# Performance work log

Hardware: AMD Instinct MI355X
Metric: run time of the kernel (lower is better)

Reference implementation:

```python
import jax, jax.numpy as jnp
import numpy as np

B, NE, NMAX = 256, 90, 270
ZE = PE = GE = PPS = 32
NPROPS = 20
FP, SGE, LATH = 256, 64, 128
PIN = FP + SGE + LATH  # 448 = pred_inp_size = conv input (add_to_node)
C1, C2, H = 448, 256, 3
P1 = P2 = 512
EPS = 1e-5

PNAMES = ['sg_emb_table','lat_W1','lat_b1','lat_bn1_g','lat_bn1_b','lat_bn1_m','lat_bn1_v',
          'lat_W2','lat_b2','lat_bn2_g','lat_bn2_b','lat_bn2_m','lat_bn2_v',
          'z_emb_table','period_table','group_table','props','W_props','b_props','W_phys','b_phys',
          'gat1_W','gat1_as','gat1_ad','gat1_b','gat2_W','gat2_as','gat2_ad','gat2_b',
          'pW1','pb1','pbn1_g','pbn1_b','pbn1_m','pbn1_v',
          'pW2','pb2','pbn2_g','pbn2_b','pbn2_m','pbn2_v','pW3','pb3']

def _bn(x, g, b, m, v):
    return (x - m) * g / jnp.sqrt(v + EPS) + b

def _lrelu(x, s=0.2):
    return jnp.where(x >= 0, x, s * x)

def _gat(x, adj, W, a_s, a_d, bias):
    # PyG DenseGATConv: concat=False (mean over heads), dropout=0, negative_slope=0.2
    Bn, N, _ = x.shape
    h = (x @ W).reshape(Bn, N, H, -1)                      # [B,N,H,C]
    asrc = (h * a_s).sum(-1)                               # [B,N,H]
    adst = (h * a_d).sum(-1)
    alpha = asrc[:, None, :, :] + adst[:, :, None, :]      # [B,i,j,H]
    alpha = _lrelu(alpha, 0.2)
    adj_sl = jnp.maximum(adj, jnp.eye(N, dtype=adj.dtype))  # add self loops
    alpha = jnp.where(adj_sl[..., None] > 0, alpha, -jnp.inf)
    alpha = jax.nn.softmax(alpha, axis=2)                  # softmax over sources j
    out = jnp.einsum('bijh,bjhc->bihc', alpha, h)
    return out.mean(2) + bias                              # [B,N,C]

def _forward(comp, sg, lat, period_idx, group_idx, p):
    sg_x = p['sg_emb_table'][sg[:, 0]]                     # [B,SGE]
    # lattice MLP: (Linear -> BN -> LeakyReLU(True)==identity) x2
    h = _bn(lat @ p['lat_W1'] + p['lat_b1'], p['lat_bn1_g'], p['lat_bn1_b'], p['lat_bn1_m'], p['lat_bn1_v'])
    lat_x = _bn(h @ p['lat_W2'] + p['lat_b2'], p['lat_bn2_g'], p['lat_bn2_b'], p['lat_bn2_m'], p['lat_bn2_v'])
    # ragged -> dense batch: expand composition counts into dense node-type grid
    n_atoms = comp.sum(1)                                  # [B]
    cum = jnp.cumsum(comp, axis=1)                         # [B,NE]
    t = jnp.arange(NMAX)
    z = jax.vmap(lambda c: jnp.searchsorted(c, t, side='right'))(cum)  # [B,NMAX]
    mask = t[None, :] < n_atoms[:, None]                   # [B,NMAX] valid nodes
    z = jnp.where(mask, z, 0)
    # PhysEmbedding: z/period/group embeddings + projected properties -> final proj
    phys = jnp.concatenate([
        p['z_emb_table'][z],
        p['period_table'][period_idx[z]],
        p['group_table'][group_idx[z]],
        p['props'][z] @ p['W_props'] + p['b_props'],
    ], axis=-1)
    phys = phys @ p['W_phys'] + p['b_phys']                # [B,NMAX,FP]
    # add_to_node: cat graph-level lat/sg embeddings onto every node, then zero-pad
    node = jnp.concatenate([
        phys,
        jnp.broadcast_to(lat_x[:, None, :], (lat_x.shape[0], NMAX, LATH)),
        jnp.broadcast_to(sg_x[:, None, :], (sg_x.shape[0], NMAX, SGE)),
    ], axis=-1)
    node = node * mask[..., None].astype(node.dtype)       # to_dense_batch zero padding
    # per-graph dense block adjacency, zero diagonal (fill_diagonal_(0))
    adj = (mask[:, :, None] & mask[:, None, :]).astype(node.dtype)
    adj = adj * (1.0 - jnp.eye(NMAX, dtype=node.dtype))
    # GNNBlock: act = LeakyReLU(True) == identity (negative_slope=1)
    x1 = _gat(node, adj, p['gat1_W'], p['gat1_as'], p['gat1_ad'], p['gat1_b'])
    x2 = _gat(x1, adj, p['gat2_W'], p['gat2_as'], p['gat2_ad'], p['gat2_b'])
    comp_x = x2.sum(1)                                     # sum over ALL NMAX slots (incl. padding, as torch does)
    feat = jnp.concatenate([comp_x, sg_x, lat_x], axis=-1) # [B,PIN]
    # prediction head (eval: dropout off, BN running stats)
    h = _lrelu(_bn(feat @ p['pW1'] + p['pb1'], p['pbn1_g'], p['pbn1_b'], p['pbn1_m'], p['pbn1_v']))
    h = _lrelu(_bn(h @ p['pW2'] + p['pb2'], p['pbn2_g'], p['pbn2_b'], p['pbn2_m'], p['pbn2_v']))
    return h @ p['pW3'] + p['pb3']                         # [B,1]

def setup_inputs():
    key = jax.random.key(0)
    ks = iter(jax.random.split(key, 64))
    def nrm(shape, s=0.05):
        return jax.random.normal(next(ks), shape, dtype=jnp.float32) * s
    comp = jax.random.randint(next(ks), (B, NE), 0, 4, dtype=jnp.int32)
    comp = comp.at[0].set(3)  # graph 0 has exactly NMAX atoms -> data N_max == NMAX
    sg = jax.random.randint(next(ks), (B, 1), 0, 230)
    lat = jax.random.uniform(next(ks), (B, 6), dtype=jnp.float32)
    period_idx = jax.random.randint(next(ks), (NE,), 0, 8)
    group_idx = jax.random.randint(next(ks), (NE,), 0, 19)
    inp = dict(comp=comp, sg=sg, lat=lat, period_idx=period_idx, group_idx=group_idx)
    inp.update(
        sg_emb_table=nrm((230, SGE)),
        lat_W1=nrm((6, LATH)), lat_b1=nrm((LATH,)),
        lat_bn1_g=jnp.ones(LATH), lat_bn1_b=jnp.zeros(LATH), lat_bn1_m=jnp.zeros(LATH), lat_bn1_v=jnp.ones(LATH),
        lat_W2=nrm((LATH, LATH)), lat_b2=nrm((LATH,)),
        lat_bn2_g=jnp.ones(LATH), lat_bn2_b=jnp.zeros(LATH), lat_bn2_m=jnp.zeros(LATH), lat_bn2_v=jnp.ones(LATH),
        z_emb_table=nrm((NE, ZE)), period_table=nrm((8, PE)), group_table=nrm((19, GE)),
        props=nrm((NE, NPROPS), 0.1), W_props=nrm((NPROPS, PPS)), b_props=nrm((PPS,)),
        W_phys=nrm((ZE + PE + GE + PPS, FP)), b_phys=nrm((FP,)),
        gat1_W=nrm((PIN, H * C1)), gat1_as=nrm((H, C1)), gat1_ad=nrm((H, C1)), gat1_b=nrm((C1,)),
        gat2_W=nrm((C1, H * C2)), gat2_as=nrm((H, C2)), gat2_ad=nrm((H, C2)), gat2_b=nrm((C2,)),
        pW1=nrm((PIN, P1)), pb1=nrm((P1,)),
        pbn1_g=jnp.ones(P1), pbn1_b=jnp.zeros(P1), pbn1_m=jnp.zeros(P1), pbn1_v=jnp.ones(P1),
        pW2=nrm((P1, P2)), pb2=nrm((P2,)),
        pbn2_g=jnp.ones(P2), pbn2_b=jnp.zeros(P2), pbn2_m=jnp.zeros(P2), pbn2_v=jnp.ones(P2),
        pW3=nrm((P2, 1)), pb3=nrm((1,)),
    )
    return inp

def reference(comp, sg, lat, period_idx, group_idx,
              sg_emb_table, lat_W1, lat_b1, lat_bn1_g, lat_bn1_b, lat_bn1_m, lat_bn1_v,
              lat_W2, lat_b2, lat_bn2_g, lat_bn2_b, lat_bn2_m, lat_bn2_v,
              z_emb_table, period_table, group_table, props, W_props, b_props, W_phys, b_phys,
              gat1_W, gat1_as, gat1_ad, gat1_b, gat2_W, gat2_as, gat2_ad, gat2_b,
              pW1, pb1, pbn1_g, pbn1_b, pbn1_m, pbn1_v,
              pW2, pb2, pbn2_g, pbn2_b, pbn2_m, pbn2_v, pW3, pb3):
    vals = (sg_emb_table, lat_W1, lat_b1, lat_bn1_g, lat_bn1_b, lat_bn1_m, lat_bn1_v,
            lat_W2, lat_b2, lat_bn2_g, lat_bn2_b, lat_bn2_m, lat_bn2_v,
            z_emb_table, period_table, group_table, props, W_props, b_props, W_phys, b_phys,
            gat1_W, gat1_as, gat1_ad, gat1_b, gat2_W, gat2_as, gat2_ad, gat2_b,
            pW1, pb1, pbn1_g, pbn1_b, pbn1_m, pbn1_v,
            pW2, pb2, pbn2_g, pbn2_b, pbn2_m, pbn2_v, pW3, pb3)
    p = dict(zip(PNAMES, vals))
    return _forward(comp, sg, lat, period_idx, group_idx, p)
```

## Files before the change

kernel.cpp:

```cpp
#include <hip/hip_runtime.h>
#include <math.h>

#define BB 256
#define NEL 90
#define NMAX 270
#define C1 448
#define C2 256
#define PIN 448
#define LATH 128
#define SGE 64
#define P1 512
#define EPSB 1e-5f

typedef short shortx8 __attribute__((ext_vector_type(8)));
typedef float floatx4 __attribute__((ext_vector_type(4)));

__device__ __forceinline__ float bf2f(unsigned short u) {
  return __uint_as_float(((unsigned)u) << 16);
}
__device__ __forceinline__ unsigned short f2bf(float f) {
  unsigned x = __float_as_uint(f);
  unsigned r = (x + 0x7fffu + ((x >> 16) & 1u)) >> 16;
  return (unsigned short)r;
}
__device__ __forceinline__ void gld16(const void* g, void* l) {
  __builtin_amdgcn_global_load_lds(
      (const __attribute__((address_space(1))) unsigned int*)g,
      (__attribute__((address_space(3))) unsigned int*)l, 16, 0, 0);
}

__global__ __launch_bounds__(256) void k_prep(
    const int* __restrict__ comp, const int* __restrict__ sg, const float* __restrict__ lat,
    const float* __restrict__ sg_emb,
    const float* __restrict__ W1, const float* __restrict__ b1,
    const float* __restrict__ g1, const float* __restrict__ be1,
    const float* __restrict__ m1, const float* __restrict__ v1,
    const float* __restrict__ W2, const float* __restrict__ b2,
    const float* __restrict__ g2, const float* __restrict__ be2,
    const float* __restrict__ m2, const float* __restrict__ v2,
    float* __restrict__ sgx, float* __restrict__ latx,
    int* __restrict__ z, int* __restrict__ natoms) {
  int b = blockIdx.x;
  int tid = threadIdx.x;
  __shared__ int cum[NEL];
  __shared__ float hbuf[LATH];
  __shared__ float latl[6];
  if (tid == 0) {
    int s = 0;
    for (int e = 0; e < NEL; ++e) { s += comp[b * NEL + e]; cum[e] = s; }
    natoms[b] = s;
  }
  if (tid < 6) latl[tid] = lat[b * 6 + tid];
  __syncthreads();
  int n = cum[NEL - 1];
  for (int t = tid; t < NMAX; t += blockDim.x) {
    int zz = -1;
    if (t < n) {
      for (int e = 0; e < NEL; ++e) { if (cum[e] > t) { zz = e; break; } }
    }
    z[b * NMAX + t] = zz;
  }
  if (tid < SGE) {
    int si = sg[b];
    sgx[b * SGE + tid] = sg_emb[si * SGE + tid];
  }
  if (tid < LATH) {
    float acc = b1[tid];
    for (int k = 0; k < 6; ++k) acc += latl[k] * W1[k * LATH + tid];
    acc = (acc - m1[tid]) * g1[tid] * rsqrtf(v1[tid] + EPSB) + be1[tid];
    hbuf[tid] = acc;
  }
  __syncthreads();
  if (tid < LATH) {
    float acc = b2[tid];
    for (int k = 0; k < LATH; ++k) acc += hbuf[k] * W2[k * LATH + tid];
    acc = (acc - m2[tid]) * g2[tid] * rsqrtf(v2[tid] + EPSB) + be2[tid];
    latx[b * LATH + tid] = acc;
  }
}

__global__ __launch_bounds__(256) void k_scan(const int* __restrict__ natoms,
                                              int* __restrict__ off,
                                              int* __restrict__ aoff,
                                              float* __restrict__ zerobuf) {
  __shared__ int sh[BB];
  int tid = threadIdx.x;
  zerobuf[tid] = 0.f;
  int v0 = natoms[tid];
  sh[tid] = v0;
  for (int d = 1; d < BB; d <<= 1) {
    __syncthreads();
    int v = (tid >= d) ? sh[tid - d] : 0;
    __syncthreads();
    sh[tid] += v;
  }
  __syncthreads();
  off[tid] = sh[tid] - v0;
  __syncthreads();
  int sz = 3 * ((((v0 + 15) >> 4) << 4)) * ((((v0 + 31) >> 5) << 5));
  sh[tid] = sz;
  for (int d = 1; d < BB; d <<= 1) {
    __syncthreads();
    int v = (tid >= d) ? sh[tid - d] : 0;
    __syncthreads();
    sh[tid] += v;
  }
  __syncthreads();
  aoff[tid] = sh[tid] - sz;
}

__global__ __launch_bounds__(256) void k_physpe(
    const int* __restrict__ period_idx, const int* __restrict__ group_idx,
    const float* __restrict__ z_emb, const float* __restrict__ period_t,
    const float* __restrict__ group_t, const float* __restrict__ props,
    const float* __restrict__ Wp, const float* __restrict__ bp,
    const float* __restrict__ Wphys, const float* __restrict__ bphys,
    float* __restrict__ physpe) {
  int e = blockIdx.x;
  int tid = threadIdx.x;
  __shared__ float ph[128];
  if (tid < 32) ph[tid] = z_emb[e * 32 + tid];
  else if (tid < 64) ph[tid] = period_t[period_idx[e] * 32 + tid - 32];
  else if (tid < 96) ph[tid] = group_t[group_idx[e] * 32 + tid - 64];
  else if (tid < 128) {
    int j = tid - 96;
    float acc = bp[j];
    for (int k = 0; k < 20; ++k) acc += props[e * 20 + k] * Wp[k * 32 + j];
    ph[tid] = acc;
  }
  __syncthreads();
  float acc = bphys[tid];
  for (int k = 0; k < 128; ++k) acc += ph[k] * Wphys[k * 256 + tid];
  physpe[e * 256 + tid] = acc;
}

__global__ __launch_bounds__(256) void k_nodep(
    const int* __restrict__ z, const int* __restrict__ off, const int* __restrict__ natoms,
    const float* __restrict__ physpe, const float* __restrict__ latx,
    const float* __restrict__ sgx, unsigned short* __restrict__ x0) {
  int b = blockIdx.x;
  int n = natoms[b], ob = off[b];
  int tid = threadIdx.x;
  __shared__ int zl[NMAX];
  for (int t = tid; t < n; t += 256) zl[t] = z[b * NMAX + t];
  __syncthreads();
  int items = n * 56;
  for (int e = tid; e < items; e += 256) {
    int t = e / 56, c8 = (e - t * 56) << 3;
    int zt = zl[t];
    float v[8];
    if (c8 < 256) {
      float4 a = *(const float4*)(physpe + zt * 256 + c8);
      float4 c = *(const float4*)(physpe + zt * 256 + c8 + 4);
      v[0] = a.x; v[1] = a.y; v[2] = a.z; v[3] = a.w;
      v[4] = c.x; v[5] = c.y; v[6] = c.z; v[7] = c.w;
    } else if (c8 < 384) {
      float4 a = *(const float4*)(latx + b * LATH + c8 - 256);
      float4 c = *(const float4*)(latx + b * LATH + c8 - 252);
      v[0] = a.x; v[1] = a.y; v[2] = a.z; v[3] = a.w;
      v[4] = c.x; v[5] = c.y; v[6] = c.z; v[7] = c.w;
    } else {
      float4 a = *(const float4*)(sgx + b * SGE + c8 - 384);
      float4 c = *(const float4*)(sgx + b * SGE + c8 - 380);
      v[0] = a.x; v[1] = a.y; v[2] = a.z; v[3] = a.w;
      v[4] = c.x; v[5] = c.y; v[6] = c.z; v[7] = c.w;
    }
    unsigned short u[8];
    #pragma unroll
    for (int i = 0; i < 8; ++i) u[i] = f2bf(v[i]);
    *(uint4*)(x0 + (size_t)(ob + t) * PIN + c8) = *(uint4*)u;
  }
}

__global__ __launch_bounds__(256) void k_wprep(
    const float* __restrict__ W, unsigned short* __restrict__ Wt, int K, int NC3) {
  int k0 = blockIdx.x << 5;
  int c0 = blockIdx.y << 5;
  __shared__ float ts[32][33];
  int e = threadIdx.x << 2;
  int kk = e >> 5, cc = e & 31;
  float4 v = *(const float4*)(W + (size_t)(k0 + kk) * NC3 + c0 + cc);
  ts[kk][cc] = v.x; ts[kk][cc + 1] = v.y; ts[kk][cc + 2] = v.z; ts[kk][cc + 3] = v.w;
  __syncthreads();
  int c2 = threadIdx.x & 31, kg = threadIdx.x >> 5;
  ushort4 u;
  u.x = f2bf(ts[kg * 4 + 0][c2]); u.y = f2bf(ts[kg * 4 + 1][c2]);
  u.z = f2bf(ts[kg * 4 + 2][c2]); u.w = f2bf(ts[kg * 4 + 3][c2]);
  *(ushort4*)(Wt + (size_t)(c0 + c2) * K + k0 + (kg << 2)) = u;
}

__global__ __launch_bounds__(64) void k_fold(
    const float* __restrict__ W, const float* __restrict__ a_s, const float* __restrict__ a_d,
    int NC3, int C, float* __restrict__ wsv, float* __restrict__ wdv) {
  int k = blockIdx.x;
  int tid = threadIdx.x;
  for (int h = 0; h < 3; ++h) {
    float ss = 0.f, sd = 0.f;
    for (int c = tid; c < C; c += 64) {
      float wv = W[(size_t)k * NC3 + h * C + c];
      ss += wv * a_s[h * C + c];
      sd += wv * a_d[h * C + c];
    }
    for (int o = 32; o > 0; o >>= 1) { ss += __shfl_down(ss, o); sd += __shfl_down(sd, o); }
    if (tid == 0) { wsv[k * 3 + h] = ss; wdv[k * 3 + h] = sd; }
  }
}

__global__ __launch_bounds__(256) void k_av2(
    const unsigned short* __restrict__ x, const float* __restrict__ wsv,
    const float* __restrict__ wdv, const int* __restrict__ off,
    const int* __restrict__ natoms, float* __restrict__ asrc,
    float* __restrict__ adst, int K) {
  __shared__ float sw[C1 * 3], dw[C1 * 3];
  int tid = threadIdx.x;
  for (int e = tid; e < K * 3; e += 256) { sw[e] = wsv[e]; dw[e] = wdv[e]; }
  __syncthreads();
  int total = off[BB - 1] + natoms[BB - 1];
  int row = blockIdx.x * 256 + tid;
  if (row >= total) return;
  const unsigned short* xr = x + (size_t)row * K;
  float s0 = 0.f, s1 = 0.f, s2 = 0.f, d0 = 0.f, d1 = 0.f, d2 = 0.f;
  for (int k = 0; k < K; k += 8) {
    uint4 raw = *(const uint4*)(xr + k);
    unsigned short us[8];
    *(uint4*)us = raw;
    #pragma unroll
    for (int u = 0; u < 8; ++u) {
      float xv = bf2f(us[u]);
      int kb = (k + u) * 3;
      s0 += xv * sw[kb + 0]; s1 += xv * sw[kb + 1]; s2 += xv * sw[kb + 2];
      d0 += xv * dw[kb + 0]; d1 += xv * dw[kb + 1]; d2 += xv * dw[kb + 2];
    }
  }
  asrc[row * 3 + 0] = s0; asrc[row * 3 + 1] = s1; asrc[row * 3 + 2] = s2;
  adst[row * 3 + 0] = d0; adst[row * 3 + 1] = d1; adst[row * 3 + 2] = d2;
}

#define MTMAX 17
__global__ __launch_bounds__(256) void k_alpha(
    const float* __restrict__ asrc, const float* __restrict__ adst,
    const int* __restrict__ off, const int* __restrict__ natoms,
    const int* __restrict__ aoff, unsigned short* __restrict__ alpha) {
  int bid = blockIdx.x;
  int b = bid & (BB - 1);
  int hm = bid >> 8;
  int h = hm % 3;
  int mt = hm / 3;
  int n = natoms[b];
  if (n == 0) return;
  int mtn = (n + 15) >> 4;
  if (mt >= mtn) return;
  int ktn = (n + 31) >> 5;
  int rext = mtn << 4, kext = ktn << 5;
  int ob = off[b];
  size_t ab = (size_t)aoff[b] + (size_t)h * rext * kext;
  int tid = threadIdx.x;
  int wv = tid >> 6, lane = tid & 63;
  __shared__ float asl[288];
  for (int j = tid; j < kext; j += 256)
    asl[j] = (j < n) ? asrc[(ob + j) * 3 + h] : 0.f;
  __syncthreads();
  #pragma unroll
  for (int r = 0; r < 4; ++r) {
    int i = (mt << 4) + (wv << 2) + r;
    unsigned short* rowp = alpha + ab + (size_t)i * kext;
    if (i >= n) {
      for (int j = lane; j < kext; j += 64) rowp[j] = 0;
      continue;
    }
    float ad = adst[(ob + i) * 3 + h];
    float m = -1e30f;
    for (int j = lane; j < n; j += 64) {
      float sc = asl[j] + ad;
      sc = fmaxf(sc, 0.2f * sc);
      m = fmaxf(m, sc);
    }
    for (int o = 32; o > 0; o >>= 1) m = fmaxf(m, __shfl_xor(m, o));
    float s = 0.f;
    for (int j = lane; j < n; j += 64) {
      float sc = asl[j] + ad;
      sc = fmaxf(sc, 0.2f * sc);
      s += __expf(sc - m);
    }
    for (int o = 32; o > 0; o >>= 1) s += __shfl_xor(s, o);
    float rs = 1.f / s;
    for (int j = lane; j < kext; j += 64) {
      float v = 0.f;
      if (j < n) {
        float sc = asl[j] + ad;
        sc = fmaxf(sc, 0.2f * sc);
        v = __expf(sc - m) * rs;
      }
      rowp[j] = f2bf(v);
    }
  }
}

#define MTW 5

__global__ __launch_bounds__(256, 2) void k_fused_mfma(
    const unsigned short* __restrict__ xin, const unsigned short* __restrict__ Wt,
    const unsigned short* __restrict__ alpha, const int* __restrict__ aoff,
    const int* __restrict__ off, const int* __restrict__ natoms,
    const float* __restrict__ bias, const float* __restrict__ zerobuf,
    unsigned short* __restrict__ xout, int K, int C, int NC) {
  int bid = blockIdx.x;
  int xg = bid & 7;
  int g = bid >> 3;
  int cblk = g % NC;
  int b = xg + ((g / NC) << 3);
  int c0 = cblk << 6;
  int n = natoms[b];
  if (n == 0) return;
  int ob = off[b];
  size_t ab = (size_t)aoff[b];
  int tid = threadIdx.x;
  int wv = tid >> 6;
  int lane = tid & 63;
  int m16 = lane & 15;
  int q = lane >> 4;

  int mtn = (n + 15) >> 4;
  int jmax = mtn << 4;
  int ktn = (n + 31) >> 5;
  int kext = ktn << 5;
  size_t hstride = (size_t)jmax * kext;

  __shared__ unsigned short xs[2][17 * 512];
  __shared__ unsigned short tt[36 * 512];

  const unsigned short* xsrc[MTW];
  #pragma unroll
  for (int t_i = 0; t_i < MTW; ++t_i) {
    int mt = wv + (t_i << 2);
    int j = (mt << 4) + m16;
    xsrc[t_i] = (j < n) ? (xin + (size_t)(ob + j) * K + (q << 3))
                        : (const unsigned short*)zerobuf;
  }

  floatx4 acc[MTW][4];
  #pragma unroll
  for (int i = 0; i < MTW; ++i)
    #pragma unroll
    for (int nt = 0; nt < 4; ++nt) acc[i][nt] = (floatx4)0.f;

  for (int h = 0; h < 3; ++h) {
    floatx4 tac[MTW][4];
    #pragma unroll
    for (int i = 0; i < MTW; ++i)
      #pragma unroll
      for (int nt = 0; nt < 4; ++nt) tac[i][nt] = (floatx4)0.f;

    const unsigned short* wsrc = Wt + (size_t)(h * C + c0 + lane) * K + (wv << 3);

    #pragma unroll
    for (int t_i = 0; t_i < MTW; ++t_i) {
      int mt = wv + (t_i << 2);
      if (mt < mtn) gld16(xsrc[t_i], &xs[0][mt << 9]);
    }
    gld16(wsrc, &tt[wv << 9]);
    __syncthreads();

    int buf = 0;
    for (int k0 = 0; k0 < K; k0 += 32) {
      int k1 = k0 + 32;
      if (k1 < K) {
        #pragma unroll
        for (int t_i = 0; t_i < MTW; ++t_i) {
          int mt = wv + (t_i << 2);
          if (mt < mtn) gld16(xsrc[t_i] + k1, &xs[buf ^ 1][mt << 9]);
        }
        gld16(wsrc + k1, &tt[((buf ^ 1) << 11) + (wv << 9)]);
      }
      const unsigned short* wb = &tt[buf << 11];
      shortx8 bfr[4];
      #pragma unroll
      for (int nt = 0; nt < 4; ++nt)
        bfr[nt] = *(const shortx8*)(wb + (q << 9) + (((nt << 4) + m16) << 3));
      #pragma unroll
      for (int t_i = 0; t_i < MTW; ++t_i) {
        int mt = wv + (t_i << 2);
        if (mt < mtn) {
          shortx8 a = *(const shortx8*)(&xs[buf][(mt << 9) + (((q << 4) + m16) << 3)]);
          #pragma unroll
          for (int nt = 0; nt < 4; ++nt)
            tac[t_i][nt] = __builtin_amdgcn_mfma_f32_16x16x32_bf16(a, bfr[nt], tac[t_i][nt], 0, 0, 0);
        }
      }
      __syncthreads();
      buf ^= 1;
    }
    #pragma unroll
    for (int t_i = 0; t_i < MTW; ++t_i) {
      int mt = wv + (t_i << 2);
      if (mt < mtn) {
        int jbase = (mt << 4) + (q << 2);
        #pragma unroll
        for (int nt = 0; nt < 4; ++nt) {
          floatx4 d = tac[t_i][nt];
          ushort4 u;
          u.x = f2bf(d.x); u.y = f2bf(d.y); u.z = f2bf(d.z); u.w = f2bf(d.w);
          int c = (nt << 4) + m16;
          *(ushort4*)(tt + ((jbase >> 3) << 9) + (c << 3) + (jbase & 7)) = u;
        }
      }
    }
    for (int e = tid; e < ((kext - jmax) << 6); e += 256) {
      int j = jmax + (e >> 6), c = e & 63;
      tt[((j >> 3) << 9) + (c << 3) + (j & 7)] = 0;
    }
    __syncthreads();
    const unsigned short* ap = alpha + ab + (size_t)h * hstride;
    for (int k0p = 0; k0p < kext; k0p += 32) {
      shortx8 tb[4];
      #pragma unroll
      for (int nt = 0; nt < 4; ++nt)
        tb[nt] = *(const shortx8*)(tt + (((k0p >> 3) + q) << 9) + (((nt << 4) + m16) << 3));
      #pragma unroll
      for (int t_i = 0; t_i < MTW; ++t_i) {
        int mt = wv + (t_i << 2);
        if (mt < mtn) {
          shortx8 af = *(const shortx8*)(ap + (size_t)((mt << 4) + m16) * kext + k0p + (q << 3));
          #pragma unroll
          for (int nt = 0; nt < 4; ++nt)
            acc[t_i][nt] = __builtin_amdgcn_mfma_f32_16x16x32_bf16(af, tb[nt], acc[t_i][nt], 0, 0, 0);
        }
      }
    }
    __syncthreads();
  }
  float bq[4];
  #pragma unroll
  for (int nt = 0; nt < 4; ++nt) bq[nt] = bias[c0 + (nt << 4) + m16];
  const float inv3 = 1.f / 3.f;
  #pragma unroll
  for (int t_i = 0; t_i < MTW; ++t_i) {
    int mt = wv + (t_i << 2);
    if (mt < mtn) {
      #pragma unroll
      for (int nt = 0; nt < 4; ++nt) {
        floatx4 d = acc[t_i][nt];
        int cidx = c0 + (nt << 4) + m16;
        #pragma unroll
        for (int r = 0; r < 4; ++r) {
          int i = (mt << 4) + (q << 2) + r;
          if (i < n) xout[(size_t)(ob + i) * C + cidx] = f2bf(d[r] * inv3 + bq[nt]);
        }
      }
    }
  }
}

__global__ __launch_bounds__(128) void k_pad(
    const float* __restrict__ b1, const float* __restrict__ W2,
    const float* __restrict__ b2g, float* __restrict__ pad2) {
  int c = blockIdx.x;
  int tid = threadIdx.x;
  float s = 0.f;
  for (int k = tid; k < C1; k += 128) {
    float bv = b1[k];
    const float* wr = W2 + (size_t)k * (3 * C2) + c;
    s += bv * (wr[0] + wr[C2] + wr[2 * C2]);
  }
  __shared__ float red[128];
  red[tid] = s;
  __syncthreads();
  for (int st = 64; st > 0; st >>= 1) {
    if (tid < st) red[tid] += red[tid + st];
    __syncthreads();
  }
  if (tid == 0) pad2[c] = red[0] * (1.f / 3.f) + b2g[c];
}

__global__ __launch_bounds__(256) void k_feat2(
    const unsigned short* __restrict__ x2, const float* __restrict__ pad2,
    const int* __restrict__ off, const int* __restrict__ natoms,
    const float* __restrict__ sgx, const float* __restrict__ latx,
    float* __restrict__ feat) {
  int b = blockIdx.y;
  int chunk = blockIdx.x;
  int tid = threadIdx.x;
  int n = natoms[b], ob = off[b];
  if (chunk == 17) {
    atomicAdd(&feat[b * PIN + tid], (float)(NMAX - n) * pad2[tid]);
    if (tid < SGE) feat[b * PIN + 256 + tid] = sgx[b * SGE + tid];
    if (tid < LATH) feat[b * PIN + 320 + tid] = latx[b * LATH + tid];
    return;
  }
  int i0 = chunk << 4;
  if (i0 >= n) return;
  int i1 = min(i0 + 16, n);
  float s = 0.f;
  for (int i = i0; i < i1; ++i) s += bf2f(x2[(size_t)(ob + i) * C2 + tid]);
  atomicAdd(&feat[b * PIN + tid], s);
}

__global__ __launch_bounds__(512) void k_head(
    const float* __restrict__ feat,
    const float* __restrict__ W1, const float* __restrict__ b1,
    const float* __restrict__ g1, const float* __restrict__ be1,
    const float* __restrict__ m1, const float* __restrict__ v1,
    const float* __restrict__ W2, const float* __restrict__ b2,
    const float* __restrict__ g2, const float* __restrict__ be2,
    const float* __restrict__ m2, const float* __restrict__ v2,
    const float* __restrict__ W3, const float* __restrict__ b3,
    float* __restrict__ out) {
  int b = blockIdx.x, tid = threadIdx.x;
  __shared__ float f[PIN];
  __shared__ float h1[P1];
  __shared__ float h2[P1];
  __shared__ float red[512];
  for (int i = tid; i < PIN; i += 512) f[i] = feat[b * PIN + i];
  __syncthreads();
  {
    int o = tid;
    float acc = b1[o];
    for (int k = 0; k < PIN; ++k) acc += f[k] * W1[k * P1 + o];
    acc = (acc - m1[o]) * g1[o] * rsqrtf(v1[o] + EPSB) + be1[o];
    h1[o] = acc >= 0.f ? acc : 0.2f * acc;
  }
  __syncthreads();
  {
    int o = tid;
    float acc = b2[o];
    for (int k = 0; k < P1; ++k) acc += h1[k] * W2[k * P1 + o];
    acc = (acc - m2[o]) * g2[o] * rsqrtf(v2[o] + EPSB) + be2[o];
    h2[o] = acc >= 0.f ? acc : 0.2f * acc;
  }
  __syncthreads();
  red[tid] = h2[tid] * W3[tid];
  __syncthreads();
  for (int s = 256; s > 0; s >>= 1) {
    if (tid < s) red[tid] += red[tid + s];
    __syncthreads();
  }
  if (tid == 0) out[b] = red[0] + b3[0];
}

extern "C" void kernel_launch(void* const* d_in, const int* in_sizes, int n_in,
                              void* d_out, int out_size, void* d_ws, size_t ws_size,
                              hipStream_t stream) {
  const int*   comp       = (const int*)d_in[0];
  const int*   sg         = (const int*)d_in[1];
  const float* lat        = (const float*)d_in[2];
  const int*   period_idx = (const int*)d_in[3];
  const int*   group_idx  = (const int*)d_in[4];
  const float* sg_emb     = (const float*)d_in[5];
  const float* lat_W1     = (const float*)d_in[6];
  const float* lat_b1     = (const float*)d_in[7];
  const float* lat_bn1_g  = (const float*)d_in[8];
  const float* lat_bn1_b  = (const float*)d_in[9];
  const float* lat_bn1_m  = (const float*)d_in[10];
  const float* lat_bn1_v  = (const float*)d_in[11];
  const float* lat_W2     = (const float*)d_in[12];
  const float* lat_b2     = (const float*)d_in[13];
  const float* lat_bn2_g  = (const float*)d_in[14];
  const float* lat_bn2_b  = (const float*)d_in[15];
  const float* lat_bn2_m  = (const float*)d_in[16];
  const float* lat_bn2_v  = (const float*)d_in[17];
  const float* z_emb      = (const float*)d_in[18];
  const float* period_t   = (const float*)d_in[19];
  const float* group_t    = (const float*)d_in[20];
  const float* props      = (const float*)d_in[21];
  const float* W_props    = (const float*)d_in[22];
  const float* b_props    = (const float*)d_in[23];
  const float* W_phys     = (const float*)d_in[24];
  const float* b_phys     = (const float*)d_in[25];
  const float* gat1_W     = (const float*)d_in[26];
  const float* gat1_as    = (const float*)d_in[27];
  const float* gat1_ad    = (const float*)d_in[28];
  const float* gat1_b     = (const float*)d_in[29];
  const float* gat2_W     = (const float*)d_in[30];
  const float* gat2_as    = (const float*)d_in[31];
  const float* gat2_ad    = (const float*)d_in[32];
  const float* gat2_b     = (const float*)d_in[33];
  const float* pW1        = (const float*)d_in[34];
  const float* pb1        = (const float*)d_in[35];
  const float* pbn1_g     = (const float*)d_in[36];
  const float* pbn1_b     = (const float*)d_in[37];
  const float* pbn1_m     = (const float*)d_in[38];
  const float* pbn1_v     = (const float*)d_in[39];
  const float* pW2        = (const float*)d_in[40];
  const float* pb2        = (const float*)d_in[41];
  const float* pbn2_g     = (const float*)d_in[42];
  const float* pbn2_b     = (const float*)d_in[43];
  const float* pbn2_m     = (const float*)d_in[44];
  const float* pbn2_v     = (const float*)d_in[45];
  const float* pW3        = (const float*)d_in[46];
  const float* pb3        = (const float*)d_in[47];

  float* ws = (float*)d_ws;
  const size_t o_sgx  = 0;
  const size_t o_latx = o_sgx  + (size_t)BB * SGE;
  const size_t o_nat  = o_latx + (size_t)BB * LATH;
  const size_t o_off  = o_nat  + BB;
  const size_t o_aoff = o_off  + BB;
  const size_t o_z    = o_aoff + BB;
  const size_t o_phys = o_z    + (size_t)BB * NMAX;
  const size_t o_wsv  = o_phys + (size_t)NEL * 256;
  const size_t o_wdv  = o_wsv  + (size_t)C1 * 3;
  const size_t o_asrc = o_wdv  + (size_t)C1 * 3;
  const size_t o_adst = o_asrc + (size_t)BB * NMAX * 3;
  const size_t o_pad2 = o_adst + (size_t)BB * NMAX * 3;
  const size_t o_zero = o_pad2 + 256;
  const size_t o_wt1  = o_zero + 256;
  const size_t o_wt2  = o_wt1  + (size_t)(3 * C1) * PIN / 2;
  const size_t o_x0   = o_wt2  + (size_t)(3 * C2) * C1 / 2;
  const size_t o_x1   = o_x0   + (size_t)BB * NMAX * PIN / 2;
  const size_t o_alph = o_x1   + (size_t)BB * NMAX * PIN / 2;

  float* sgx    = ws + o_sgx;
  float* latx   = ws + o_latx;
  int*   natoms = (int*)(ws + o_nat);
  int*   off    = (int*)(ws + o_off);
  int*   aoff   = (int*)(ws + o_aoff);
  int*   z      = (int*)(ws + o_z);
  float* physpe = ws + o_phys;
  float* wsv    = ws + o_wsv;
  float* wdv    = ws + o_wdv;
  float* asrc   = ws + o_asrc;
  float* adst   = ws + o_adst;
  float* pad2   = ws + o_pad2;
  float* zerobuf = ws + o_zero;
  unsigned short* wt1   = (unsigned short*)(ws + o_wt1);
  unsigned short* wt2   = (unsigned short*)(ws + o_wt2);
  unsigned short* x0    = (unsigned short*)(ws + o_x0);
  unsigned short* x1    = (unsigned short*)(ws + o_x1);
  unsigned short* x2    = x0;
  unsigned short* alpha = (unsigned short*)(ws + o_alph);
  float* feat   = ws + o_x1;

  const int AVG = (BB * NMAX + 255) / 256;
  const int ALG = BB * 3 * MTMAX;

  k_prep<<<BB, 256, 0, stream>>>(comp, sg, lat, sg_emb,
      lat_W1, lat_b1, lat_bn1_g, lat_bn1_b, lat_bn1_m, lat_bn1_v,
      lat_W2, lat_b2, lat_bn2_g, lat_bn2_b, lat_bn2_m, lat_bn2_v,
      sgx, latx, z, natoms);
  k_scan<<<1, 256, 0, stream>>>(natoms, off, aoff, zerobuf);
  k_physpe<<<NEL, 256, 0, stream>>>(period_idx, group_idx, z_emb, period_t, group_t,
      props, W_props, b_props, W_phys, b_phys, physpe);
  k_nodep<<<BB, 256, 0, stream>>>(z, off, natoms, physpe, latx, sgx, x0);

  k_wprep<<<dim3(PIN / 32, (3 * C1) / 32), 256, 0, stream>>>(gat1_W, wt1, PIN, 3 * C1);
  k_wprep<<<dim3(C1 / 32, (3 * C2) / 32), 256, 0, stream>>>(gat2_W, wt2, C1, 3 * C2);
  k_pad<<<256, 128, 0, stream>>>(gat1_b, gat2_W, gat2_b, pad2);

  k_fold<<<C1, 64, 0, stream>>>(gat1_W, gat1_as, gat1_ad, 3 * C1, C1, wsv, wdv);
  k_av2<<<AVG, 256, 0, stream>>>(x0, wsv, wdv, off, natoms, asrc, adst, PIN);
  k_alpha<<<ALG, 256, 0, stream>>>(asrc, adst, off, natoms, aoff, alpha);
  k_fused_mfma<<<(C1 / 64) * BB, 256, 0, stream>>>(x0, wt1, alpha, aoff,
      off, natoms, gat1_b, zerobuf, x1, PIN, C1, C1 / 64);

  k_fold<<<C1, 64, 0, stream>>>(gat2_W, gat2_as, gat2_ad, 3 * C2, C2, wsv, wdv);
  k_av2<<<AVG, 256, 0, stream>>>(x1, wsv, wdv, off, natoms, asrc, adst, C1);
  k_alpha<<<ALG, 256, 0, stream>>>(asrc, adst, off, natoms, aoff, alpha);
  k_fused_mfma<<<(C2 / 64) * BB, 256, 0, stream>>>(x1, wt2, alpha, aoff,
      off, natoms, gat2_b, zerobuf, x2, C1, C2, C2 / 64);

  hipMemsetAsync(feat, 0, (size_t)BB * PIN * sizeof(float), stream);
  k_feat2<<<dim3(18, BB), 256, 0, stream>>>(x2, pad2, off, natoms, sgx, latx, feat);
  k_head<<<BB, 512, 0, stream>>>(feat,
      pW1, pb1, pbn1_g, pbn1_b, pbn1_m, pbn1_v,
      pW2, pb2, pbn2_g, pbn2_b, pbn2_m, pbn2_v,
      pW3, pb3, (float*)d_out);
}
```

Baseline: 753.6 us.

## Merge setup kernels into one launch and make k_av2 wave-per-row

Combines the prep, scan, physics-embedding, weight-transpose, attention-fold and bias-pad kernels into one block-indexed setup kernel. This removes several small launches and the serial gaps between them, and keeps separate fold buffers for both GAT layers. The scan block now recomputes natoms from comp, so it no longer depends on the prep blocks. k_av2 switches from one thread per row to one wavefront per row with coalesced 16-byte loads and a shuffle reduction, over a fixed grid of 1024 blocks. The cost is a larger kernel with branchy roles and more register and shared-memory pressure.

```diff
diff --git a/kernel.cpp b/kernel.cpp
--- a/kernel.cpp
+++ b/kernel.cpp
@@ -29,109 +29,177 @@
       (__attribute__((address_space(3))) unsigned int*)l, 16, 0, 0);
 }
 
-__global__ __launch_bounds__(256) void k_prep(
+#define NB_PREP  BB
+#define NB_SCAN  1
+#define NB_PHYS  NEL
+#define NB_WP1   (14 * 42)
+#define NB_WP2   (14 * 24)
+#define NB_FOLD  112
+#define NB_PAD   64
+#define SETUP_GRID (NB_PREP + NB_SCAN + NB_PHYS + NB_WP1 + NB_WP2 + 2 * NB_FOLD + NB_PAD)
+
+__global__ __launch_bounds__(256) void k_setup(
     const int* __restrict__ comp, const int* __restrict__ sg, const float* __restrict__ lat,
     const float* __restrict__ sg_emb,
-    const float* __restrict__ W1, const float* __restrict__ b1,
-    const float* __restrict__ g1, const float* __restrict__ be1,
-    const float* __restrict__ m1, const float* __restrict__ v1,
-    const float* __restrict__ W2, const float* __restrict__ b2,
-    const float* __restrict__ g2, const float* __restrict__ be2,
-    const float* __restrict__ m2, const float* __restrict__ v2,
-    float* __restrict__ sgx, float* __restrict__ latx,
-    int* __restrict__ z, int* __restrict__ natoms) {
-  int b = blockIdx.x;
-  int tid = threadIdx.x;
-  __shared__ int cum[NEL];
-  __shared__ float hbuf[LATH];
-  __shared__ float latl[6];
-  if (tid == 0) {
-    int s = 0;
-    for (int e = 0; e < NEL; ++e) { s += comp[b * NEL + e]; cum[e] = s; }
-    natoms[b] = s;
-  }
-  if (tid < 6) latl[tid] = lat[b * 6 + tid];
-  __syncthreads();
-  int n = cum[NEL - 1];
-  for (int t = tid; t < NMAX; t += blockDim.x) {
-    int zz = -1;
-    if (t < n) {
-      for (int e = 0; e < NEL; ++e) { if (cum[e] > t) { zz = e; break; } }
-    }
-    z[b * NMAX + t] = zz;
-  }
-  if (tid < SGE) {
-    int si = sg[b];
-    sgx[b * SGE + tid] = sg_emb[si * SGE + tid];
-  }
-  if (tid < LATH) {
-    float acc = b1[tid];
-    for (int k = 0; k < 6; ++k) acc += latl[k] * W1[k * LATH + tid];
-    acc = (acc - m1[tid]) * g1[tid] * rsqrtf(v1[tid] + EPSB) + be1[tid];
-    hbuf[tid] = acc;
-  }
-  __syncthreads();
-  if (tid < LATH) {
-    float acc = b2[tid];
-    for (int k = 0; k < LATH; ++k) acc += hbuf[k] * W2[k * LATH + tid];
-    acc = (acc - m2[tid]) * g2[tid] * rsqrtf(v2[tid] + EPSB) + be2[tid];
-    latx[b * LATH + tid] = acc;
-  }
-}
-
-__global__ __launch_bounds__(256) void k_scan(const int* __restrict__ natoms,
-                                              int* __restrict__ off,
-                                              int* __restrict__ aoff,
-                                              float* __restrict__ zerobuf) {
-  __shared__ int sh[BB];
-  int tid = threadIdx.x;
-  zerobuf[tid] = 0.f;
-  int v0 = natoms[tid];
-  sh[tid] = v0;
-  for (int d = 1; d < BB; d <<= 1) {
-    __syncthreads();
-    int v = (tid >= d) ? sh[tid - d] : 0;
-    __syncthreads();
-    sh[tid] += v;
-  }
-  __syncthreads();
-  off[tid] = sh[tid] - v0;
-  __syncthreads();
-  int sz = 3 * ((((v0 + 15) >> 4) << 4)) * ((((v0 + 31) >> 5) << 5));
-  sh[tid] = sz;
-  for (int d = 1; d < BB; d <<= 1) {
-    __syncthreads();
-    int v = (tid >= d) ? sh[tid - d] : 0;
-    __syncthreads();
-    sh[tid] += v;
-  }
-  __syncthreads();
-  aoff[tid] = sh[tid] - sz;
-}
-
-__global__ __launch_bounds__(256) void k_physpe(
+    const float* __restrict__ lW1, const float* __restrict__ lb1,
+    const float* __restrict__ lg1, const float* __restrict__ lbe1,
+    const float* __restrict__ lm1, const float* __restrict__ lv1,
+    const float* __restrict__ lW2, const float* __restrict__ lb2,
+    const float* __restrict__ lg2, const float* __restrict__ lbe2,
+    const float* __restrict__ lm2, const float* __restrict__ lv2,
     const int* __restrict__ period_idx, const int* __restrict__ group_idx,
     const float* __restrict__ z_emb, const float* __restrict__ period_t,
     const float* __restrict__ group_t, const float* __restrict__ props,
     const float* __restrict__ Wp, const float* __restrict__ bp,
     const float* __restrict__ Wphys, const float* __restrict__ bphys,
-    float* __restrict__ physpe) {
-  int e = blockIdx.x;
+    const float* __restrict__ gat1_W, const float* __restrict__ gat1_as,
+    const float* __restrict__ gat1_ad, const float* __restrict__ gat1_b,
+    const float* __restrict__ gat2_W, const float* __restrict__ gat2_as,
+    const float* __restrict__ gat2_ad, const float* __restrict__ gat2_b,
+    float* __restrict__ sgx, float* __restrict__ latx, int* __restrict__ z,
+    int* __restrict__ natoms, int* __restrict__ off, int* __restrict__ aoff,
+    float* __restrict__ zerobuf, float* __restrict__ physpe,
+    unsigned short* __restrict__ wt1, unsigned short* __restrict__ wt2,
+    float* __restrict__ wsv1, float* __restrict__ wdv1,
+    float* __restrict__ wsv2, float* __restrict__ wdv2, float* __restrict__ pad2) {
+  int r = blockIdx.x;
   int tid = threadIdx.x;
-  __shared__ float ph[128];
-  if (tid < 32) ph[tid] = z_emb[e * 32 + tid];
-  else if (tid < 64) ph[tid] = period_t[period_idx[e] * 32 + tid - 32];
-  else if (tid < 96) ph[tid] = group_t[group_idx[e] * 32 + tid - 64];
-  else if (tid < 128) {
-    int j = tid - 96;
-    float acc = bp[j];
-    for (int k = 0; k < 20; ++k) acc += props[e * 20 + k] * Wp[k * 32 + j];
-    ph[tid] = acc;
-  }
-  __syncthreads();
-  float acc = bphys[tid];
-  for (int k = 0; k < 128; ++k) acc += ph[k] * Wphys[k * 256 + tid];
-  physpe[e * 256 + tid] = acc;
+  int wv = tid >> 6, lane = tid & 63;
+
+  if (r < NB_PREP) {
+    int b = r;
+    __shared__ int cum[NEL];
+    __shared__ float hbuf[LATH];
+    __shared__ float latl[6];
+    if (tid == 0) {
+      int s = 0;
+      for (int e = 0; e < NEL; ++e) { s += comp[b * NEL + e]; cum[e] = s; }
+    }
+    if (tid < 6) latl[tid] = lat[b * 6 + tid];
+    __syncthreads();
+    int n = cum[NEL - 1];
+    for (int t = tid; t < NMAX; t += 256) {
+      int zz = -1;
+      if (t < n) {
+        for (int e = 0; e < NEL; ++e) { if (cum[e] > t) { zz = e; break; } }
+      }
+      z[b * NMAX + t] = zz;
+    }
+    if (tid < SGE) sgx[b * SGE + tid] = sg_emb[sg[b] * SGE + tid];
+    if (tid < LATH) {
+      float acc = lb1[tid];
+      for (int k = 0; k < 6; ++k) acc += latl[k] * lW1[k * LATH + tid];
+      acc = (acc - lm1[tid]) * lg1[tid] * rsqrtf(lv1[tid] + EPSB) + lbe1[tid];
+      hbuf[tid] = acc;
+    }
+    __syncthreads();
+    if (tid < LATH) {
+      float acc = lb2[tid];
+      for (int k = 0; k < LATH; ++k) acc += hbuf[k] * lW2[k * LATH + tid];
+      acc = (acc - lm2[tid]) * lg2[tid] * rsqrtf(lv2[tid] + EPSB) + lbe2[tid];
+      latx[b * LATH + tid] = acc;
+    }
+    return;
+  }
+  r -= NB_PREP;
+  if (r < NB_SCAN) {
+    __shared__ int sh[BB];
+    zerobuf[tid] = 0.f;
+    int v0 = 0;
+    for (int e = 0; e < NEL; ++e) v0 += comp[tid * NEL + e];
+    natoms[tid] = v0;
+    sh[tid] = v0;
+    for (int d = 1; d < BB; d <<= 1) {
+      __syncthreads();
+      int v = (tid >= d) ? sh[tid - d] : 0;
+      __syncthreads();
+      sh[tid] += v;
+    }
+    __syncthreads();
+    off[tid] = sh[tid] - v0;
+    __syncthreads();
+    int sz = 3 * ((((v0 + 15) >> 4) << 4)) * ((((v0 + 31) >> 5) << 5));
+    sh[tid] = sz;
+    for (int d = 1; d < BB; d <<= 1) {
+      __syncthreads();
+      int v = (tid >= d) ? sh[tid - d] : 0;
+      __syncthreads();
+      sh[tid] += v;
+    }
+    __syncthreads();
+    aoff[tid] = sh[tid] - sz;
+    return;
+  }
+  r -= NB_SCAN;
+  if (r < NB_PHYS) {
+    int e = r;
+    __shared__ float ph[128];
+    if (tid < 32) ph[tid] = z_emb[e * 32 + tid];
+    else if (tid < 64) ph[tid] = period_t[period_idx[e] * 32 + tid - 32];
+    else if (tid < 96) ph[tid] = group_t[group_idx[e] * 32 + tid - 64];
+    else if (tid < 128) {
+      int j = tid - 96;
+      float acc = bp[j];
+      for (int k = 0; k < 20; ++k) acc += props[e * 20 + k] * Wp[k * 32 + j];
+      ph[tid] = acc;
+    }
+    __syncthreads();
+    float acc = bphys[tid];
+    for (int k = 0; k < 128; ++k) acc += ph[k] * Wphys[k * 256 + tid];
+    physpe[e * 256 + tid] = acc;
+    return;
+  }
+  r -= NB_PHYS;
+  if (r < NB_WP1 + NB_WP2) {
+    const float* W;
+    unsigned short* Wt;
+    int NC3, bx, by;
+    if (r < NB_WP1) { W = gat1_W; Wt = wt1; NC3 = 3 * C1; bx = r % 14; by = r / 14; }
+    else { int r2 = r - NB_WP1; W = gat2_W; Wt = wt2; NC3 = 3 * C2; bx = r2 % 14; by = r2 / 14; }
+    int k0 = bx << 5, c0 = by << 5;
+    __shared__ float ts[32][33];
+    int e4 = tid << 2;
+    int kk = e4 >> 5, cc = e4 & 31;
+    float4 v = *(const float4*)(W + (size_t)(k0 + kk) * NC3 + c0 + cc);
+    ts[kk][cc] = v.x; ts[kk][cc + 1] = v.y; ts[kk][cc + 2] = v.z; ts[kk][cc + 3] = v.w;
+    __syncthreads();
+    int c2 = tid & 31, kg = tid >> 5;
+    ushort4 u;
+    u.x = f2bf(ts[kg * 4 + 0][c2]); u.y = f2bf(ts[kg * 4 + 1][c2]);
+    u.z = f2bf(ts[kg * 4 + 2][c2]); u.w = f2bf(ts[kg * 4 + 3][c2]);
+    *(ushort4*)(Wt + (size_t)(c0 + c2) * 448 + k0 + (kg << 2)) = u;
+    return;
+  }
+  r -= NB_WP1 + NB_WP2;
+  if (r < 2 * NB_FOLD) {
+    const float* W; const float* as_; const float* ad_;
+    float* wsv; float* wdv; int NC3, C, kb;
+    if (r < NB_FOLD) { W = gat1_W; as_ = gat1_as; ad_ = gat1_ad; wsv = wsv1; wdv = wdv1; NC3 = 3 * C1; C = C1; kb = r << 2; }
+    else { int r2 = r - NB_FOLD; W = gat2_W; as_ = gat2_as; ad_ = gat2_ad; wsv = wsv2; wdv = wdv2; NC3 = 3 * C2; C = C2; kb = r2 << 2; }
+    int k = kb + wv;
+    for (int h = 0; h < 3; ++h) {
+      float ss = 0.f, sd = 0.f;
+      for (int c = lane; c < C; c += 64) {
+        float wvv = W[(size_t)k * NC3 + h * C + c];
+        ss += wvv * as_[h * C + c];
+        sd += wvv * ad_[h * C + c];
+      }
+      for (int o = 32; o > 0; o >>= 1) { ss += __shfl_xor(ss, o); sd += __shfl_xor(sd, o); }
+      if (lane == 0) { wsv[k * 3 + h] = ss; wdv[k * 3 + h] = sd; }
+    }
+    return;
+  }
+  r -= 2 * NB_FOLD;
+  {
+    int c = (r << 2) + wv;
+    float s = 0.f;
+    for (int k = lane; k < C1; k += 64) {
+      const float* wr = gat2_W + (size_t)k * (3 * C2) + c;
+      s += gat1_b[k] * (wr[0] + wr[C2] + wr[2 * C2]);
+    }
+    for (int o = 32; o > 0; o >>= 1) s += __shfl_xor(s, o);
+    if (lane == 0) pad2[c] = s * (1.f / 3.f) + gat2_b[c];
+  }
 }
 
 __global__ __launch_bounds__(256) void k_nodep(
@@ -172,40 +240,6 @@
   }
 }
 
-__global__ __launch_bounds__(256) void k_wprep(
-    const float* __restrict__ W, unsigned short* __restrict__ Wt, int K, int NC3) {
-  int k0 = blockIdx.x << 5;
-  int c0 = blockIdx.y << 5;
-  __shared__ float ts[32][33];
-  int e = threadIdx.x << 2;
-  int kk = e >> 5, cc = e & 31;
-  float4 v = *(const float4*)(W + (size_t)(k0 + kk) * NC3 + c0 + cc);
-  ts[kk][cc] = v.x; ts[kk][cc + 1] = v.y; ts[kk][cc + 2] = v.z; ts[kk][cc + 3] = v.w;
-  __syncthreads();
-  int c2 = threadIdx.x & 31, kg = threadIdx.x >> 5;
-  ushort4 u;
-  u.x = f2bf(ts[kg * 4 + 0][c2]); u.y = f2bf(ts[kg * 4 + 1][c2]);
-  u.z = f2bf(ts[kg * 4 + 2][c2]); u.w = f2bf(ts[kg * 4 + 3][c2]);
-  *(ushort4*)(Wt + (size_t)(c0 + c2) * K + k0 + (kg << 2)) = u;
-}
-
-__global__ __launch_bounds__(64) void k_fold(
-    const float* __restrict__ W, const float* __restrict__ a_s, const float* __restrict__ a_d,
-    int NC3, int C, float* __restrict__ wsv, float* __restrict__ wdv) {
-  int k = blockIdx.x;
-  int tid = threadIdx.x;
-  for (int h = 0; h < 3; ++h) {
-    float ss = 0.f, sd = 0.f;
-    for (int c = tid; c < C; c += 64) {
-      float wv = W[(size_t)k * NC3 + h * C + c];
-      ss += wv * a_s[h * C + c];
-      sd += wv * a_d[h * C + c];
-    }
-    for (int o = 32; o > 0; o >>= 1) { ss += __shfl_down(ss, o); sd += __shfl_down(sd, o); }
-    if (tid == 0) { wsv[k * 3 + h] = ss; wdv[k * 3 + h] = sd; }
-  }
-}
-
 __global__ __launch_bounds__(256) void k_av2(
     const unsigned short* __restrict__ x, const float* __restrict__ wsv,
     const float* __restrict__ wdv, const int* __restrict__ off,
@@ -216,24 +250,33 @@
   for (int e = tid; e < K * 3; e += 256) { sw[e] = wsv[e]; dw[e] = wdv[e]; }
   __syncthreads();
   int total = off[BB - 1] + natoms[BB - 1];
-  int row = blockIdx.x * 256 + tid;
-  if (row >= total) return;
-  const unsigned short* xr = x + (size_t)row * K;
-  float s0 = 0.f, s1 = 0.f, s2 = 0.f, d0 = 0.f, d1 = 0.f, d2 = 0.f;
-  for (int k = 0; k < K; k += 8) {
-    uint4 raw = *(const uint4*)(xr + k);
-    unsigned short us[8];
-    *(uint4*)us = raw;
+  int wv = tid >> 6, lane = tid & 63;
+  int nk8 = K >> 3;
+  int stride = gridDim.x << 2;
+  for (int row = (blockIdx.x << 2) + wv; row < total; row += stride) {
+    float s0 = 0.f, s1 = 0.f, s2 = 0.f, d0 = 0.f, d1 = 0.f, d2 = 0.f;
+    if (lane < nk8) {
+      uint4 raw = *(const uint4*)(x + (size_t)row * K + (lane << 3));
+      unsigned short us[8];
+      *(uint4*)us = raw;
+      #pragma unroll
+      for (int u = 0; u < 8; ++u) {
+        float xv = bf2f(us[u]);
+        int kb = ((lane << 3) + u) * 3;
+        s0 += xv * sw[kb + 0]; s1 += xv * sw[kb + 1]; s2 += xv * sw[kb + 2];
+        d0 += xv * dw[kb + 0]; d1 += xv * dw[kb + 1]; d2 += xv * dw[kb + 2];
+      }
+    }
     #pragma unroll
-    for (int u = 0; u < 8; ++u) {
-      float xv = bf2f(us[u]);
-      int kb = (k + u) * 3;
-      s0 += xv * sw[kb + 0]; s1 += xv * sw[kb + 1]; s2 += xv * sw[kb + 2];
-      d0 += xv * dw[kb + 0]; d1 += xv * dw[kb + 1]; d2 += xv * dw[kb + 2];
-    }
-  }
-  asrc[row * 3 + 0] = s0; asrc[row * 3 + 1] = s1; asrc[row * 3 + 2] = s2;
-  adst[row * 3 + 0] = d0; adst[row * 3 + 1] = d1; adst[row * 3 + 2] = d2;
+    for (int o = 32; o > 0; o >>= 1) {
+      s0 += __shfl_xor(s0, o); s1 += __shfl_xor(s1, o); s2 += __shfl_xor(s2, o);
+      d0 += __shfl_xor(d0, o); d1 += __shfl_xor(d1, o); d2 += __shfl_xor(d2, o);
+    }
+    if (lane == 0) {
+      asrc[row * 3 + 0] = s0; asrc[row * 3 + 1] = s1; asrc[row * 3 + 2] = s2;
+      adst[row * 3 + 0] = d0; adst[row * 3 + 1] = d1; adst[row * 3 + 2] = d2;
+    }
+  }
 }
 
 #define MTMAX 17
@@ -449,27 +492,6 @@
       }
     }
   }
-}
-
-__global__ __launch_bounds__(128) void k_pad(
-    const float* __restrict__ b1, const float* __restrict__ W2,
-    const float* __restrict__ b2g, float* __restrict__ pad2) {
-  int c = blockIdx.x;
-  int tid = threadIdx.x;
-  float s = 0.f;
-  for (int k = tid; k < C1; k += 128) {
-    float bv = b1[k];
-    const float* wr = W2 + (size_t)k * (3 * C2) + c;
-    s += bv * (wr[0] + wr[C2] + wr[2 * C2]);
-  }
-  __shared__ float red[128];
-  red[tid] = s;
-  __syncthreads();
-  for (int st = 64; st > 0; st >>= 1) {
-    if (tid < st) red[tid] += red[tid + st];
-    __syncthreads();
-  }
-  if (tid == 0) pad2[c] = red[0] * (1.f / 3.f) + b2g[c];
 }
 
 __global__ __launch_bounds__(256) void k_feat2(
@@ -597,9 +619,11 @@
   const size_t o_aoff = o_off  + BB;
   const size_t o_z    = o_aoff + BB;
   const size_t o_phys = o_z    + (size_t)BB * NMAX;
-  const size_t o_wsv  = o_phys + (size_t)NEL * 256;
-  const size_t o_wdv  = o_wsv  + (size_t)C1 * 3;
-  const size_t o_asrc = o_wdv  + (size_t)C1 * 3;
+  const size_t o_wsv1 = o_phys + (size_t)NEL * 256;
+  const size_t o_wdv1 = o_wsv1 + (size_t)C1 * 3;
+  const size_t o_wsv2 = o_wdv1 + (size_t)C1 * 3;
+  const size_t o_wdv2 = o_wsv2 + (size_t)C1 * 3;
+  const size_t o_asrc = o_wdv2 + (size_t)C1 * 3;
   const size_t o_adst = o_asrc + (size_t)BB * NMAX * 3;
   const size_t o_pad2 = o_adst + (size_t)BB * NMAX * 3;
   const size_t o_zero = o_pad2 + 256;
@@ -616,8 +640,10 @@
   int*   aoff   = (int*)(ws + o_aoff);
   int*   z      = (int*)(ws + o_z);
   float* physpe = ws + o_phys;
-  float* wsv    = ws + o_wsv;
-  float* wdv    = ws + o_wdv;
+  float* wsv1   = ws + o_wsv1;
+  float* wdv1   = ws + o_wdv1;
+  float* wsv2   = ws + o_wsv2;
+  float* wdv2   = ws + o_wdv2;
   float* asrc   = ws + o_asrc;
   float* adst   = ws + o_adst;
   float* pad2   = ws + o_pad2;
@@ -630,30 +656,27 @@
   unsigned short* alpha = (unsigned short*)(ws + o_alph);
   float* feat   = ws + o_x1;
 
-  const int AVG = (BB * NMAX + 255) / 256;
   const int ALG = BB * 3 * MTMAX;
 
-  k_prep<<<BB, 256, 0, stream>>>(comp, sg, lat, sg_emb,
+  k_setup<<<SETUP_GRID, 256, 0, stream>>>(
+      comp, sg, lat, sg_emb,
       lat_W1, lat_b1, lat_bn1_g, lat_bn1_b, lat_bn1_m, lat_bn1_v,
       lat_W2, lat_b2, lat_bn2_g, lat_bn2_b, lat_bn2_m, lat_bn2_v,
-      sgx, latx, z, natoms);
-  k_scan<<<1, 256, 0, stream>>>(natoms, off, aoff, zerobuf);
-  k_physpe<<<NEL, 256, 0, stream>>>(period_idx, group_idx, z_emb, period_t, group_t,
-      props, W_props, b_props, W_phys, b_phys, physpe);
+      period_idx, group_idx, z_emb, period_t, group_t, props,
+      W_props, b_props, W_phys, b_phys,
+      gat1_W, gat1_as, gat1_ad, gat1_b,
+      gat2_W, gat2_as, gat2_ad, gat2_b,
+      sgx, latx, z, natoms, off, aoff, zerobuf, physpe,
+      wt1, wt2, wsv1, wdv1, wsv2, wdv2, pad2);
+
   k_nodep<<<BB, 256, 0, stream>>>(z, off, natoms, physpe, latx, sgx, x0);
 
-  k_wprep<<<dim3(PIN / 32, (3 * C1) / 32), 256, 0, stream>>>(gat1_W, wt1, PIN, 3 * C1);
-  k_wprep<<<dim3(C1 / 32, (3 * C2) / 32), 256, 0, stream>>>(gat2_W, wt2, C1, 3 * C2);
-  k_pad<<<256, 128, 0, stream>>>(gat1_b, gat2_W, gat2_b, pad2);
-
-  k_fold<<<C1, 64, 0, stream>>>(gat1_W, gat1_as, gat1_ad, 3 * C1, C1, wsv, wdv);
-  k_av2<<<AVG, 256, 0, stream>>>(x0, wsv, wdv, off, natoms, asrc, adst, PIN);
+  k_av2<<<1024, 256, 0, stream>>>(x0, wsv1, wdv1, off, natoms, asrc, adst, PIN);
   k_alpha<<<ALG, 256, 0, stream>>>(asrc, adst, off, natoms, aoff, alpha);
   k_fused_mfma<<<(C1 / 64) * BB, 256, 0, stream>>>(x0, wt1, alpha, aoff,
       off, natoms, gat1_b, zerobuf, x1, PIN, C1, C1 / 64);
 
-  k_fold<<<C1, 64, 0, stream>>>(gat2_W, gat2_as, gat2_ad, 3 * C2, C2, wsv, wdv);
-  k_av2<<<AVG, 256, 0, stream>>>(x1, wsv, wdv, off, natoms, asrc, adst, C1);
+  k_av2<<<1024, 256, 0, stream>>>(x1, wsv2, wdv2, off, natoms, asrc, adst, C1);
   k_alpha<<<ALG, 256, 0, stream>>>(asrc, adst, off, natoms, aoff, alpha);
   k_fused_mfma<<<(C2 / 64) * BB, 256, 0, stream>>>(x1, wt2, alpha, aoff,
       off, natoms, gat2_b, zerobuf, x2, C1, C2, C2 / 64);
```

New measurement: 747.0 us. No clear change (-0.9%).
